# Optimization experiments

Measured on AMD Instinct MI355X. Metric: run time of the kernel, lower is better.

## Reference

```python
import jax, jax.numpy as jnp
import numpy as np

EPSILON = 0.1        # SinkhornConfig.epsilon
NUM_INNER_ITER = 10  # SinkhornConfig.num_inner_iter
STAB = 1e-8          # denominator stabilizer from forward()


def setup_inputs() -> dict:
    key = jax.random.key(0)
    k1, k2 = jax.random.split(key)
    source_features = jax.random.uniform(k1, (8192, 64), dtype=jnp.float32)
    target_features = jax.random.uniform(k2, (8192, 64), dtype=jnp.float32)
    return {"source_features": source_features, "target_features": target_features}


def _cost_matrix(s, t):
    # pairwise Euclidean distance ||s_i - t_j||_2, computed without the
    # [Ns, Nt, D] broadcast the torch code materializes (same math).
    s2 = jnp.sum(s * s, axis=1, keepdims=True)          # [Ns, 1]
    t2 = jnp.sum(t * t, axis=1, keepdims=True).T        # [1, Nt]
    sq = s2 + t2 - 2.0 * (s @ t.T)                      # [Ns, Nt]
    return jnp.sqrt(jnp.maximum(sq, 0.0))


def reference(source_features, target_features):
    ns = source_features.shape[0]
    nt = target_features.shape[0]
    # uniform weights, normalized (source_weights/target_weights is None path)
    sw = jnp.full((ns, 1), 1.0 / ns, dtype=source_features.dtype)
    tw = jnp.full((nt, 1), 1.0 / nt, dtype=target_features.dtype)

    cost = _cost_matrix(source_features, target_features)   # [Ns, Nt]
    kernel = jnp.exp(-cost / EPSILON)                        # Gibbs kernel

    u = jnp.ones((ns, 1), dtype=cost.dtype)
    v = jnp.ones((nt, 1), dtype=cost.dtype)
    for _ in range(NUM_INNER_ITER):  # fixed small trip count
        u = sw / (kernel @ v + STAB)
        v = tw / (kernel.T @ u + STAB)

    coupling = u * kernel * v.T                              # [Ns, Nt]
    sinkhorn_dist = jnp.sum(coupling * cost) / (ns * nt)     # reduction='mean'
    return sinkhorn_dist, coupling, u, v
```

## Files before the change

kernel.cpp:

```cpp
#include <hip/hip_runtime.h>
#include <hip/hip_bf16.h>
#include <math.h>

#define NSRC 8192
#define NTGT 8192
#define DIM 64

typedef short bf16x8 __attribute__((ext_vector_type(8)));
typedef float f32x16 __attribute__((ext_vector_type(16)));

__device__ __forceinline__ float wave_reduce_sum(float x) {
#pragma unroll
  for (int off = 32; off > 0; off >>= 1) x += __shfl_down(x, off, 64);
  return x;
}

__device__ __forceinline__ float bflo(unsigned int u) {
  return __uint_as_float(u << 16);
}
__device__ __forceinline__ float bfhi(unsigned int u) {
  return __uint_as_float(u & 0xFFFF0000u);
}
__device__ __forceinline__ unsigned short f2bfr(float x) {
  __hip_bfloat16 b = __float2bfloat16(x);
  return __hip_bfloat16_raw(b).x;
}

__global__ __launch_bounds__(256) void norms_k(const float* __restrict__ S,
                                               const float* __restrict__ T,
                                               float* __restrict__ s2,
                                               float* __restrict__ t2) {
  int i = blockIdx.x * 256 + threadIdx.x;
  if (i >= NSRC + NTGT) return;
  const float* base = (i < NSRC) ? (S + (size_t)i * DIM)
                                 : (T + (size_t)(i - NSRC) * DIM);
  const float4* p = (const float4*)base;
  float a = 0.f;
#pragma unroll
  for (int k = 0; k < DIM / 4; ++k) {
    float4 v = p[k];
    a += v.x * v.x + v.y * v.y + v.z * v.z + v.w * v.w;
  }
  if (i < NSRC) s2[i] = a;
  else          t2[i - NSRC] = a;
}

__global__ __launch_bounds__(256) void prep_k(const float* __restrict__ S,
                                              const float* __restrict__ T,
                                              unsigned short* __restrict__ Shi,
                                              unsigned short* __restrict__ Slo,
                                              unsigned short* __restrict__ Thi,
                                              unsigned short* __restrict__ Tlo) {
  int i = blockIdx.x * 256 + threadIdx.x;
  const float* src;
  unsigned short *dh, *dl;
  if (i < 65536) { src = S; dh = Shi; dl = Slo; }
  else { src = T; dh = Thi; dl = Tlo; i -= 65536; }
  const float4* p = (const float4*)(src + (size_t)i * 8);
  float4 x = p[0], y = p[1];
  float vals[8] = {x.x, x.y, x.z, x.w, y.x, y.y, y.z, y.w};
  unsigned int h[8], lo[8];
#pragma unroll
  for (int e = 0; e < 8; ++e) {
    unsigned short hr = f2bfr(vals[e]);
    h[e] = hr;
    lo[e] = f2bfr(vals[e] - bflo(hr));
  }
  uint4 hw = make_uint4(h[0] | (h[1] << 16), h[2] | (h[3] << 16),
                        h[4] | (h[5] << 16), h[6] | (h[7] << 16));
  uint4 lw = make_uint4(lo[0] | (lo[1] << 16), lo[2] | (lo[3] << 16),
                        lo[4] | (lo[5] << 16), lo[6] | (lo[7] << 16));
  *(uint4*)(dh + (size_t)i * 8) = hw;
  *(uint4*)(dl + (size_t)i * 8) = lw;
}

__global__ __launch_bounds__(256) void init_k(float* __restrict__ c,
                                              float* __restrict__ v_out,
                                              float* __restrict__ rowacc) {
  int i = blockIdx.x * 256 + threadIdx.x;
  if (i < NTGT) {
    c[i] = 0.f;
    v_out[i] = 1.f;
    rowacc[i] = 0.f;
  }
}

#define PR(r) ((((r) >> 3) + (((r)&7) << 3)))

__global__ __launch_bounds__(256) void kbuild_mfma_k(
    const unsigned short* __restrict__ Shi, const unsigned short* __restrict__ Slo,
    const unsigned short* __restrict__ Thi, const unsigned short* __restrict__ Tlo,
    const float* __restrict__ s2, const float* __restrict__ t2,
    __hip_bfloat16* __restrict__ Kb, __hip_bfloat16* __restrict__ KbT,
    float* __restrict__ rowacc) {
  __shared__ unsigned short sAh[64][72], sAl[64][72];
  __shared__ unsigned short sBh[64][72], sBl[64][72];
  __shared__ unsigned short stage[64][72];
  __shared__ float sS2[64], sT2[64];

  const int tid = threadIdx.x;
  const int bm = blockIdx.y * 64, bn = blockIdx.x * 64;

#pragma unroll
  for (int p = 0; p < 2; ++p) {
    int f = tid + 256 * p;
    int row = f >> 3, seg = (f & 7) * 8;
    *(uint4*)&sAh[row][seg] = ((const uint4*)(Shi + (size_t)bm * DIM))[f];
    *(uint4*)&sAl[row][seg] = ((const uint4*)(Slo + (size_t)bm * DIM))[f];
    *(uint4*)&sBh[row][seg] = ((const uint4*)(Thi + (size_t)bn * DIM))[f];
    *(uint4*)&sBl[row][seg] = ((const uint4*)(Tlo + (size_t)bn * DIM))[f];
  }
  if (tid < 64) sS2[tid] = s2[bm + tid];
  else if (tid < 128) sT2[tid - 64] = t2[bn + (tid - 64)];
  __syncthreads();

  const int w = tid >> 6, l = tid & 63;
  const int wr = w >> 1, wc = w & 1;
  const int arow = 32 * wr + (l & 31);
  const int brow = 32 * wc + (l & 31);
  const int kh = 8 * (l >> 5);

  f32x16 acc;
#pragma unroll
  for (int i = 0; i < 16; ++i) acc[i] = 0.f;

#pragma unroll
  for (int ks = 0; ks < 4; ++ks) {
    int ko = 16 * ks + kh;
    bf16x8 ah = *(const bf16x8*)&sAh[arow][ko];
    bf16x8 al = *(const bf16x8*)&sAl[arow][ko];
    bf16x8 bh = *(const bf16x8*)&sBh[brow][ko];
    bf16x8 bl = *(const bf16x8*)&sBl[brow][ko];
    acc = __builtin_amdgcn_mfma_f32_32x32x16_bf16(ah, bh, acc, 0, 0, 0);
    acc = __builtin_amdgcn_mfma_f32_32x32x16_bf16(ah, bl, acc, 0, 0, 0);
    acc = __builtin_amdgcn_mfma_f32_32x32x16_bf16(al, bh, acc, 0, 0, 0);
  }

#pragma unroll
  for (int j = 0; j < 16; ++j) {
    int rl = (j & 3) + 8 * (j >> 2) + 4 * (l >> 5);
    int row = 32 * wr + rl, col = 32 * wc + (l & 31);
    float sq = sS2[row] + sT2[col] - 2.f * acc[j];
    float kv = __expf(-10.f * sqrtf(fmaxf(sq, 0.f)));
    stage[PR(row)][col] = f2bfr(kv);
  }
  __syncthreads();

  {
    int row = tid >> 2, q = tid & 3;
    float a = 0.f;
#pragma unroll
    for (int m = 0; m < 16; ++m)
      a += bflo((unsigned int)stage[PR(row)][16 * q + m]);
    a += __shfl_down(a, 1, 4);
    a += __shfl_down(a, 2, 4);
    if (q == 0) atomicAdd(&rowacc[bm + row], a);
  }

#pragma unroll
  for (int p = 0; p < 2; ++p) {
    int f = tid + 256 * p;
    int row = f >> 3, seg = (f & 7) * 8;
    *(uint4*)(Kb + (size_t)(bm + row) * NTGT + bn + seg) =
        *(const uint4*)&stage[PR(row)][seg];
  }
#pragma unroll
  for (int p = 0; p < 2; ++p) {
    int f = tid + 256 * p;
    int tcol = f >> 3, gro = f & 7;
    unsigned int wds[4];
#pragma unroll
    for (int e = 0; e < 4; ++e) {
      unsigned int a0 = stage[gro + 8 * (2 * e)][tcol];
      unsigned int a1 = stage[gro + 8 * (2 * e + 1)][tcol];
      wds[e] = a0 | (a1 << 16);
    }
    *(uint4*)(KbT + (size_t)(bn + tcol) * NSRC + bm + 8 * gro) =
        make_uint4(wds[0], wds[1], wds[2], wds[3]);
  }
}

__global__ __launch_bounds__(256) void initu_k(const float* __restrict__ rowacc,
                                               float* __restrict__ u) {
  int i = blockIdx.x * 256 + threadIdx.x;
  u[i] = (1.0f / NSRC) / (rowacc[i] + 1e-8f);
}

__global__ __launch_bounds__(256) void rowsum_k(const unsigned short* __restrict__ P,
                                                const float* __restrict__ x,
                                                float* __restrict__ y) {
  int row = blockIdx.x * 4 + (threadIdx.x >> 6);
  int lane = threadIdx.x & 63;
  const uint4* r4 = (const uint4*)(P + (size_t)row * NTGT);
  const float4* x4 = (const float4*)x;
  float a = 0.f;
#pragma unroll 4
  for (int s = lane; s < NTGT / 8; s += 64) {
    uint4 q = r4[s];
    float4 xa = x4[2 * s], xb = x4[2 * s + 1];
    a += bflo(q.x) * xa.x + bfhi(q.x) * xa.y
       + bflo(q.y) * xa.z + bfhi(q.y) * xa.w
       + bflo(q.z) * xb.x + bfhi(q.z) * xb.y
       + bflo(q.w) * xb.z + bfhi(q.w) * xb.w;
  }
  a = wave_reduce_sum(a);
  if (lane == 0) y[row] = (1.0f / 8192.0f) / (a + 1e-8f);
}

__global__ __launch_bounds__(256) void coupling_bf16_k(
    const unsigned short* __restrict__ Kb,
    const float* __restrict__ u,
    const float* __restrict__ v,
    float* __restrict__ C,
    float* __restrict__ partials) {
  __shared__ float red[4];
  size_t g = (size_t)blockIdx.x * 256 + threadIdx.x;
  size_t base = g * 32;
  int i = (int)(base >> 13);
  int j0 = (int)(base & 8191);
  float ui = u[i];
  const uint4* kp = (const uint4*)(Kb + base);
  const float4* vp = (const float4*)(v + j0);
  float part = 0.f;
#pragma unroll
  for (int s = 0; s < 4; ++s) {
    uint4 q = kp[s];
    float4 va = vp[2 * s], vb = vp[2 * s + 1];
    float k0 = bflo(q.x), k1 = bfhi(q.x), k2 = bflo(q.y), k3 = bfhi(q.y);
    float k4 = bflo(q.z), k5 = bfhi(q.z), k6 = bflo(q.w), k7 = bfhi(q.w);
    float c0 = ui * k0 * va.x, c1 = ui * k1 * va.y;
    float c2 = ui * k2 * va.z, c3 = ui * k3 * va.w;
    float c4 = ui * k4 * vb.x, c5 = ui * k5 * vb.y;
    float c6 = ui * k6 * vb.z, c7 = ui * k7 * vb.w;
    part += c0 * __logf(fmaxf(k0, 1e-37f)) + c1 * __logf(fmaxf(k1, 1e-37f)) +
            c2 * __logf(fmaxf(k2, 1e-37f)) + c3 * __logf(fmaxf(k3, 1e-37f)) +
            c4 * __logf(fmaxf(k4, 1e-37f)) + c5 * __logf(fmaxf(k5, 1e-37f)) +
            c6 * __logf(fmaxf(k6, 1e-37f)) + c7 * __logf(fmaxf(k7, 1e-37f));
    float* cw = C + base + 8 * s;
    *(float4*)cw       = make_float4(c0, c1, c2, c3);
    *(float4*)(cw + 4) = make_float4(c4, c5, c6, c7);
  }
  part = wave_reduce_sum(part);
  int wid = threadIdx.x >> 6, lane = threadIdx.x & 63;
  if (lane == 0) red[wid] = part;
  __syncthreads();
  if (threadIdx.x == 0)
    partials[blockIdx.x] = red[0] + red[1] + red[2] + red[3];
}

#define BM 64
#define BN 128
__global__ __launch_bounds__(256) void kbuild_k(const float* __restrict__ S,
                                                const float* __restrict__ T,
                                                const float* __restrict__ s2,
                                                const float* __restrict__ t2,
                                                float* __restrict__ Kf) {
  __shared__ float sT[BM][68];
  __shared__ float tT[BN][68];
  const int bn = blockIdx.x * BN;
  const int bm = blockIdx.y * BM;
  const int tid = threadIdx.x;
  {
    const float4* sg = (const float4*)(S + (size_t)bm * DIM);
#pragma unroll
    for (int k = 0; k < 4; ++k) {
      int f = tid + 256 * k;
      int row = f >> 4, c4 = f & 15;
      *(float4*)&sT[row][c4 * 4] = sg[f];
    }
    const float4* tg = (const float4*)(T + (size_t)bn * DIM);
#pragma unroll
    for (int k = 0; k < 8; ++k) {
      int f = tid + 256 * k;
      int row = f >> 4, c4 = f & 15;
      *(float4*)&tT[row][c4 * 4] = tg[f];
    }
  }
  __syncthreads();
  const int tx = tid & 15;
  const int ty = tid >> 4;
  float acc[4][8];
#pragma unroll
  for (int a = 0; a < 4; ++a)
#pragma unroll
    for (int b = 0; b < 8; ++b) acc[a][b] = 0.f;
  for (int k = 0; k < DIM; k += 4) {
    float4 sr[4], trg[8];
#pragma unroll
    for (int a = 0; a < 4; ++a) sr[a] = *(float4*)&sT[ty + 16 * a][k];
#pragma unroll
    for (int b = 0; b < 8; ++b) trg[b] = *(float4*)&tT[tx + 16 * b][k];
#pragma unroll
    for (int a = 0; a < 4; ++a)
#pragma unroll
      for (int b = 0; b < 8; ++b) {
        acc[a][b] += sr[a].x * trg[b].x;
        acc[a][b] += sr[a].y * trg[b].y;
        acc[a][b] += sr[a].z * trg[b].z;
        acc[a][b] += sr[a].w * trg[b].w;
      }
  }
#pragma unroll
  for (int a = 0; a < 4; ++a) {
    int gi = bm + ty + 16 * a;
    float s2v = s2[gi];
#pragma unroll
    for (int b = 0; b < 8; ++b) {
      int gj = bn + tx + 16 * b;
      float sq = s2v + t2[gj] - 2.f * acc[a][b];
      float cost = sqrtf(fmaxf(sq, 0.f));
      Kf[(size_t)gi * NTGT + gj] = __expf(-10.f * cost);
    }
  }
}

__global__ __launch_bounds__(256) void rowsum_f32_k(const float* __restrict__ K,
                                                    const float* __restrict__ v,
                                                    float* __restrict__ u_out) {
  int row = (blockIdx.x * 256 + threadIdx.x) >> 6;
  int lane = threadIdx.x & 63;
  const float4* r4 = (const float4*)(K + (size_t)row * NTGT);
  const float4* v4 = (const float4*)v;
  float a = 0.f;
#pragma unroll 4
  for (int j = lane; j < NTGT / 4; j += 64) {
    float4 k4 = r4[j];
    float4 vv = v4[j];
    a += k4.x * vv.x + k4.y * vv.y + k4.z * vv.z + k4.w * vv.w;
  }
  a = wave_reduce_sum(a);
  if (lane == 0) u_out[row] = (1.0f / NSRC) / (a + 1e-8f);
}

__global__ __launch_bounds__(256) void colsum_f32_k(const float* __restrict__ K,
                                                    const float* __restrict__ u,
                                                    float* __restrict__ c) {
  int j = blockIdx.x * 1024 + threadIdx.x * 4;
  int i0 = blockIdx.y * 64;
  float a0 = 0.f, a1 = 0.f, a2 = 0.f, a3 = 0.f;
#pragma unroll 8
  for (int i = i0; i < i0 + 64; ++i) {
    float ui = u[i];
    float4 k4 = *(const float4*)(K + (size_t)i * NTGT + j);
    a0 += k4.x * ui; a1 += k4.y * ui; a2 += k4.z * ui; a3 += k4.w * ui;
  }
  atomicAdd(&c[j + 0], a0);
  atomicAdd(&c[j + 1], a1);
  atomicAdd(&c[j + 2], a2);
  atomicAdd(&c[j + 3], a3);
}

__global__ __launch_bounds__(256) void finishv_k(float* __restrict__ c,
                                                 float* __restrict__ v_out) {
  int j = blockIdx.x * 256 + threadIdx.x;
  v_out[j] = (1.0f / NTGT) / (c[j] + 1e-8f);
  c[j] = 0.f;
}

__global__ __launch_bounds__(256) void coupling_f32_k(float* __restrict__ K,
                                                      const float* __restrict__ u,
                                                      const float* __restrict__ v,
                                                      float* __restrict__ partials) {
  __shared__ float red[4];
  size_t t0 = (size_t)blockIdx.x * 2048 + threadIdx.x;
  float part = 0.f;
#pragma unroll
  for (int s = 0; s < 8; ++s) {
    size_t f4 = t0 + (size_t)s * 256;
    size_t base = f4 * 4;
    int i = (int)(base >> 13);
    int j = (int)(base & 8191);
    float4 k4 = *(float4*)(K + base);
    float ui = u[i];
    float4 vv = *(const float4*)(v + j);
    float c0 = ui * k4.x * vv.x;
    float c1 = ui * k4.y * vv.y;
    float c2 = ui * k4.z * vv.z;
    float c3 = ui * k4.w * vv.w;
    part += c0 * __logf(k4.x) + c1 * __logf(k4.y) +
            c2 * __logf(k4.z) + c3 * __logf(k4.w);
    *(float4*)(K + base) = make_float4(c0, c1, c2, c3);
  }
  part = wave_reduce_sum(part);
  int wid = threadIdx.x >> 6, lane = threadIdx.x & 63;
  if (lane == 0) red[wid] = part;
  __syncthreads();
  if (threadIdx.x == 0)
    partials[blockIdx.x] = red[0] + red[1] + red[2] + red[3];
}

__global__ __launch_bounds__(256) void finalize_k(const float* __restrict__ partials,
                                                  float* __restrict__ out) {
  __shared__ float red[4];
  float a = 0.f;
  for (int i = threadIdx.x; i < 8192; i += 256) a += partials[i];
  a = wave_reduce_sum(a);
  int wid = threadIdx.x >> 6, lane = threadIdx.x & 63;
  if (lane == 0) red[wid] = a;
  __syncthreads();
  if (threadIdx.x == 0)
    out[0] = (red[0] + red[1] + red[2] + red[3]) *
             (-0.1f / ((float)NSRC * (float)NTGT));
}

extern "C" void kernel_launch(void* const* d_in, const int* in_sizes, int n_in,
                              void* d_out, int out_size, void* d_ws, size_t ws_size,
                              hipStream_t stream) {
  const float* S = (const float*)d_in[0];
  const float* T = (const float*)d_in[1];
  float* out = (float*)d_out;

  float* C  = out + 1;
  float* u  = out + 1 + (size_t)NSRC * NTGT;
  float* vv = u + NSRC;

  __hip_bfloat16* KbT = (__hip_bfloat16*)C;

  char* wsb = (char*)d_ws;
  float* s2       = (float*)(wsb);
  float* t2       = (float*)(wsb + (32 << 10));
  float* partials = (float*)(wsb + (64 << 10));
  float* c        = (float*)(wsb + (96 << 10));
  float* rowacc   = (float*)(wsb + (128 << 10));
  unsigned short* Shi = (unsigned short*)(wsb + (1 << 20));
  unsigned short* Slo = (unsigned short*)(wsb + (2 << 20));
  unsigned short* Thi = (unsigned short*)(wsb + (3 << 20));
  unsigned short* Tlo = (unsigned short*)(wsb + (4 << 20));
  const size_t KB_OFF = (size_t)8 << 20;
  const size_t KB_BYTES = (size_t)NSRC * NTGT * 2;
  __hip_bfloat16* Kb = (__hip_bfloat16*)(wsb + KB_OFF);

  bool full = ws_size >= KB_OFF + KB_BYTES;

  norms_k<<<(NSRC + NTGT + 255) / 256, 256, 0, stream>>>(S, T, s2, t2);

  if (full) {
    prep_k<<<512, 256, 0, stream>>>(S, T, Shi, Slo, Thi, Tlo);
    init_k<<<NTGT / 256, 256, 0, stream>>>(c, vv, rowacc);
    kbuild_mfma_k<<<dim3(128, 128), 256, 0, stream>>>(
        Shi, Slo, Thi, Tlo, s2, t2, Kb, KbT, rowacc);
    initu_k<<<NSRC / 256, 256, 0, stream>>>(rowacc, u);
    for (int it = 0; it < 10; ++it) {
      if (it > 0)
        rowsum_k<<<NSRC / 4, 256, 0, stream>>>((const unsigned short*)Kb, vv, u);
      rowsum_k<<<NTGT / 4, 256, 0, stream>>>((const unsigned short*)KbT, u, vv);
    }
    coupling_bf16_k<<<8192, 256, 0, stream>>>(
        (const unsigned short*)Kb, u, vv, C, partials);
  } else {
    init_k<<<NTGT / 256, 256, 0, stream>>>(c, vv, partials );
    kbuild_k<<<dim3(NTGT / BN, NSRC / BM), 256, 0, stream>>>(S, T, s2, t2, C);
    for (int it = 0; it < 10; ++it) {
      rowsum_f32_k<<<NSRC * 64 / 256, 256, 0, stream>>>(C, vv, u);
      colsum_f32_k<<<dim3(8, 128), 256, 0, stream>>>(C, u, c);
      finishv_k<<<NTGT / 256, 256, 0, stream>>>(c, vv);
    }
    coupling_f32_k<<<8192, 256, 0, stream>>>(C, u, vv, partials);
  }
  finalize_k<<<1, 256, 0, stream>>>(partials, out);
}
```

Before: 686.2 us.

## Drop transposed bf16 kernel copy; compute column sums from Kb with split partials

The Gibbs kernel is no longer stored a second time in transposed form. The v-update now reads the row-major Kb directly: colsum_part_k writes per-16-row-chunk column partials and csum1v_k reduces the 512 partials into v. Row sums from the build kernel are written as per-block partials instead of atomics, and the workspace layout is changed to hold the partial buffers. This removes 128MB of transposed writes and the strided LDS transpose, but each iteration now writes and reads a 16MB partial buffer.

```diff
diff --git a/kernel.cpp b/kernel.cpp
--- a/kernel.cpp
+++ b/kernel.cpp
@@ -75,24 +75,19 @@
 }
 
 __global__ __launch_bounds__(256) void init_k(float* __restrict__ c,
-                                              float* __restrict__ v_out,
-                                              float* __restrict__ rowacc) {
+                                              float* __restrict__ v_out) {
   int i = blockIdx.x * 256 + threadIdx.x;
   if (i < NTGT) {
     c[i] = 0.f;
     v_out[i] = 1.f;
-    rowacc[i] = 0.f;
-  }
-}
-
-#define PR(r) ((((r) >> 3) + (((r)&7) << 3)))
+  }
+}
 
 __global__ __launch_bounds__(256) void kbuild_mfma_k(
     const unsigned short* __restrict__ Shi, const unsigned short* __restrict__ Slo,
     const unsigned short* __restrict__ Thi, const unsigned short* __restrict__ Tlo,
     const float* __restrict__ s2, const float* __restrict__ t2,
-    __hip_bfloat16* __restrict__ Kb, __hip_bfloat16* __restrict__ KbT,
-    float* __restrict__ rowacc) {
+    __hip_bfloat16* __restrict__ Kb, float* __restrict__ rowpart) {
   __shared__ unsigned short sAh[64][72], sAl[64][72];
   __shared__ unsigned short sBh[64][72], sBl[64][72];
   __shared__ unsigned short stage[64][72];
@@ -142,7 +137,7 @@
     int row = 32 * wr + rl, col = 32 * wc + (l & 31);
     float sq = sS2[row] + sT2[col] - 2.f * acc[j];
     float kv = __expf(-10.f * sqrtf(fmaxf(sq, 0.f)));
-    stage[PR(row)][col] = f2bfr(kv);
+    stage[row][col] = f2bfr(kv);
   }
   __syncthreads();
 
@@ -151,10 +146,10 @@
     float a = 0.f;
 #pragma unroll
     for (int m = 0; m < 16; ++m)
-      a += bflo((unsigned int)stage[PR(row)][16 * q + m]);
+      a += bflo((unsigned int)stage[row][16 * q + m]);
     a += __shfl_down(a, 1, 4);
     a += __shfl_down(a, 2, 4);
-    if (q == 0) atomicAdd(&rowacc[bm + row], a);
+    if (q == 0) rowpart[(size_t)blockIdx.x * NSRC + bm + row] = a;
   }
 
 #pragma unroll
@@ -162,28 +157,17 @@
     int f = tid + 256 * p;
     int row = f >> 3, seg = (f & 7) * 8;
     *(uint4*)(Kb + (size_t)(bm + row) * NTGT + bn + seg) =
-        *(const uint4*)&stage[PR(row)][seg];
-  }
-#pragma unroll
-  for (int p = 0; p < 2; ++p) {
-    int f = tid + 256 * p;
-    int tcol = f >> 3, gro = f & 7;
-    unsigned int wds[4];
-#pragma unroll
-    for (int e = 0; e < 4; ++e) {
-      unsigned int a0 = stage[gro + 8 * (2 * e)][tcol];
-      unsigned int a1 = stage[gro + 8 * (2 * e + 1)][tcol];
-      wds[e] = a0 | (a1 << 16);
-    }
-    *(uint4*)(KbT + (size_t)(bn + tcol) * NSRC + bm + 8 * gro) =
-        make_uint4(wds[0], wds[1], wds[2], wds[3]);
-  }
-}
-
-__global__ __launch_bounds__(256) void initu_k(const float* __restrict__ rowacc,
+        *(const uint4*)&stage[row][seg];
+  }
+}
+
+__global__ __launch_bounds__(256) void initu_k(const float* __restrict__ rowpart,
                                                float* __restrict__ u) {
   int i = blockIdx.x * 256 + threadIdx.x;
-  u[i] = (1.0f / NSRC) / (rowacc[i] + 1e-8f);
+  float a = 0.f;
+#pragma unroll 8
+  for (int bn = 0; bn < 128; ++bn) a += rowpart[(size_t)bn * NSRC + i];
+  u[i] = (1.0f / NSRC) / (a + 1e-8f);
 }
 
 __global__ __launch_bounds__(256) void rowsum_k(const unsigned short* __restrict__ P,
@@ -207,6 +191,62 @@
   if (lane == 0) y[row] = (1.0f / 8192.0f) / (a + 1e-8f);
 }
 
+__global__ __launch_bounds__(256) void colsum_part_k(
+    const unsigned short* __restrict__ Kb,
+    const float* __restrict__ u,
+    float* __restrict__ c_part) {
+  const int ic = blockIdx.x;
+  const int t = threadIdx.x;
+  const uint4* kp = (const uint4*)(Kb + (size_t)ic * 16 * NTGT);
+
+  float acc[32];
+#pragma unroll
+  for (int k = 0; k < 32; ++k) acc[k] = 0.f;
+
+#pragma unroll 4
+  for (int r = 0; r < 16; ++r) {
+    float ui = u[16 * ic + r];
+    uint4 q0 = kp[r * 1024 + 0 * 256 + t];
+    uint4 q1 = kp[r * 1024 + 1 * 256 + t];
+    uint4 q2 = kp[r * 1024 + 2 * 256 + t];
+    uint4 q3 = kp[r * 1024 + 3 * 256 + t];
+    acc[0]  += bflo(q0.x) * ui; acc[1]  += bfhi(q0.x) * ui;
+    acc[2]  += bflo(q0.y) * ui; acc[3]  += bfhi(q0.y) * ui;
+    acc[4]  += bflo(q0.z) * ui; acc[5]  += bfhi(q0.z) * ui;
+    acc[6]  += bflo(q0.w) * ui; acc[7]  += bfhi(q0.w) * ui;
+    acc[8]  += bflo(q1.x) * ui; acc[9]  += bfhi(q1.x) * ui;
+    acc[10] += bflo(q1.y) * ui; acc[11] += bfhi(q1.y) * ui;
+    acc[12] += bflo(q1.z) * ui; acc[13] += bfhi(q1.z) * ui;
+    acc[14] += bflo(q1.w) * ui; acc[15] += bfhi(q1.w) * ui;
+    acc[16] += bflo(q2.x) * ui; acc[17] += bfhi(q2.x) * ui;
+    acc[18] += bflo(q2.y) * ui; acc[19] += bfhi(q2.y) * ui;
+    acc[20] += bflo(q2.z) * ui; acc[21] += bfhi(q2.z) * ui;
+    acc[22] += bflo(q2.w) * ui; acc[23] += bfhi(q2.w) * ui;
+    acc[24] += bflo(q3.x) * ui; acc[25] += bfhi(q3.x) * ui;
+    acc[26] += bflo(q3.y) * ui; acc[27] += bfhi(q3.y) * ui;
+    acc[28] += bflo(q3.z) * ui; acc[29] += bfhi(q3.z) * ui;
+    acc[30] += bflo(q3.w) * ui; acc[31] += bfhi(q3.w) * ui;
+  }
+
+  float* dst = c_part + (size_t)ic * NTGT + 8 * t;
+#pragma unroll
+  for (int s = 0; s < 4; ++s) {
+    *(float4*)(dst + 2048 * s)     = make_float4(acc[8 * s + 0], acc[8 * s + 1],
+                                                 acc[8 * s + 2], acc[8 * s + 3]);
+    *(float4*)(dst + 2048 * s + 4) = make_float4(acc[8 * s + 4], acc[8 * s + 5],
+                                                 acc[8 * s + 6], acc[8 * s + 7]);
+  }
+}
+
+__global__ __launch_bounds__(256) void csum1v_k(const float* __restrict__ c_part,
+                                                float* __restrict__ v_out) {
+  int j = blockIdx.x * 256 + threadIdx.x;
+  float a = 0.f;
+#pragma unroll 8
+  for (int ic = 0; ic < 512; ++ic) a += c_part[(size_t)ic * NTGT + j];
+  v_out[j] = (1.0f / NTGT) / (a + 1e-8f);
+}
+
 __global__ __launch_bounds__(256) void coupling_bf16_k(
     const unsigned short* __restrict__ Kb,
     const float* __restrict__ u,
@@ -414,41 +454,42 @@
   float* u  = out + 1 + (size_t)NSRC * NTGT;
   float* vv = u + NSRC;
 
-  __hip_bfloat16* KbT = (__hip_bfloat16*)C;
-
   char* wsb = (char*)d_ws;
   float* s2       = (float*)(wsb);
   float* t2       = (float*)(wsb + (32 << 10));
   float* partials = (float*)(wsb + (64 << 10));
   float* c        = (float*)(wsb + (96 << 10));
-  float* rowacc   = (float*)(wsb + (128 << 10));
-  unsigned short* Shi = (unsigned short*)(wsb + (1 << 20));
-  unsigned short* Slo = (unsigned short*)(wsb + (2 << 20));
-  unsigned short* Thi = (unsigned short*)(wsb + (3 << 20));
-  unsigned short* Tlo = (unsigned short*)(wsb + (4 << 20));
-  const size_t KB_OFF = (size_t)8 << 20;
+  const size_t KB_OFF = 512 << 10;
   const size_t KB_BYTES = (size_t)NSRC * NTGT * 2;
+  const size_t CP_OFF = KB_OFF + KB_BYTES;
+  const size_t CP_BYTES = (size_t)512 * NTGT * 4;
   __hip_bfloat16* Kb = (__hip_bfloat16*)(wsb + KB_OFF);
-
-  bool full = ws_size >= KB_OFF + KB_BYTES;
+  float* c_part = (float*)(wsb + CP_OFF);
+  unsigned short* Shi = (unsigned short*)(wsb + CP_OFF);
+  unsigned short* Slo = (unsigned short*)(wsb + CP_OFF + (1 << 20));
+  unsigned short* Thi = (unsigned short*)(wsb + CP_OFF + (2 << 20));
+  unsigned short* Tlo = (unsigned short*)(wsb + CP_OFF + (3 << 20));
+  float* rowpart = (float*)(wsb + CP_OFF + (4 << 20));
+
+  bool full = ws_size >= CP_OFF + CP_BYTES;
 
   norms_k<<<(NSRC + NTGT + 255) / 256, 256, 0, stream>>>(S, T, s2, t2);
+  init_k<<<NTGT / 256, 256, 0, stream>>>(c, vv);
 
   if (full) {
     prep_k<<<512, 256, 0, stream>>>(S, T, Shi, Slo, Thi, Tlo);
-    init_k<<<NTGT / 256, 256, 0, stream>>>(c, vv, rowacc);
     kbuild_mfma_k<<<dim3(128, 128), 256, 0, stream>>>(
-        Shi, Slo, Thi, Tlo, s2, t2, Kb, KbT, rowacc);
-    initu_k<<<NSRC / 256, 256, 0, stream>>>(rowacc, u);
+        Shi, Slo, Thi, Tlo, s2, t2, Kb, rowpart);
+    initu_k<<<NSRC / 256, 256, 0, stream>>>(rowpart, u);
     for (int it = 0; it < 10; ++it) {
       if (it > 0)
         rowsum_k<<<NSRC / 4, 256, 0, stream>>>((const unsigned short*)Kb, vv, u);
-      rowsum_k<<<NTGT / 4, 256, 0, stream>>>((const unsigned short*)KbT, u, vv);
+      colsum_part_k<<<512, 256, 0, stream>>>((const unsigned short*)Kb, u, c_part);
+      csum1v_k<<<NTGT / 256, 256, 0, stream>>>(c_part, vv);
     }
     coupling_bf16_k<<<8192, 256, 0, stream>>>(
         (const unsigned short*)Kb, u, vv, C, partials);
   } else {
-    init_k<<<NTGT / 256, 256, 0, stream>>>(c, vv, partials );
     kbuild_k<<<dim3(NTGT / BN, NSRC / BM), 256, 0, stream>>>(S, T, s2, t2, C);
     for (int it = 0; it < 10; ++it) {
       rowsum_f32_k<<<NSRC * 64 / 256, 256, 0, stream>>>(C, vv, u);
```

Result: slower. 860.7 us (+25.4%).

## Recompute cost via MFMA in coupling pass and replace row-sum atomics with partials

Applied to the files above, without the earlier changes.

The coupling kernel no longer reads the stored bf16 Gibbs matrix. It recomputes the distance tile with split-bf16 MFMA and writes the coupling and the cost-weighted partial sums directly. This removes a full read of the large matrix at the price of extra matrix math per tile. The row-sum atomics in the kernel build are replaced by per-block partial writes that initu_k reduces, which also drops the init launch. The rowsum unroll factor goes from 4 to 8.

```diff
diff --git a/kernel.cpp b/kernel.cpp
--- a/kernel.cpp
+++ b/kernel.cpp
@@ -75,13 +75,11 @@
 }
 
 __global__ __launch_bounds__(256) void init_k(float* __restrict__ c,
-                                              float* __restrict__ v_out,
-                                              float* __restrict__ rowacc) {
+                                              float* __restrict__ v_out) {
   int i = blockIdx.x * 256 + threadIdx.x;
   if (i < NTGT) {
     c[i] = 0.f;
     v_out[i] = 1.f;
-    rowacc[i] = 0.f;
   }
 }
 
@@ -92,7 +90,7 @@
     const unsigned short* __restrict__ Thi, const unsigned short* __restrict__ Tlo,
     const float* __restrict__ s2, const float* __restrict__ t2,
     __hip_bfloat16* __restrict__ Kb, __hip_bfloat16* __restrict__ KbT,
-    float* __restrict__ rowacc) {
+    float* __restrict__ rowpart) {
   __shared__ unsigned short sAh[64][72], sAl[64][72];
   __shared__ unsigned short sBh[64][72], sBl[64][72];
   __shared__ unsigned short stage[64][72];
@@ -154,7 +152,7 @@
       a += bflo((unsigned int)stage[PR(row)][16 * q + m]);
     a += __shfl_down(a, 1, 4);
     a += __shfl_down(a, 2, 4);
-    if (q == 0) atomicAdd(&rowacc[bm + row], a);
+    if (q == 0) rowpart[(size_t)blockIdx.x * NSRC + bm + row] = a;
   }
 
 #pragma unroll
@@ -180,10 +178,13 @@
   }
 }
 
-__global__ __launch_bounds__(256) void initu_k(const float* __restrict__ rowacc,
+__global__ __launch_bounds__(256) void initu_k(const float* __restrict__ rowpart,
                                                float* __restrict__ u) {
   int i = blockIdx.x * 256 + threadIdx.x;
-  u[i] = (1.0f / NSRC) / (rowacc[i] + 1e-8f);
+  float a = 0.f;
+#pragma unroll 8
+  for (int bn = 0; bn < 128; ++bn) a += rowpart[(size_t)bn * NSRC + i];
+  u[i] = (1.0f / NSRC) / (a + 1e-8f);
 }
 
 __global__ __launch_bounds__(256) void rowsum_k(const unsigned short* __restrict__ P,
@@ -194,7 +195,7 @@
   const uint4* r4 = (const uint4*)(P + (size_t)row * NTGT);
   const float4* x4 = (const float4*)x;
   float a = 0.f;
-#pragma unroll 4
+#pragma unroll 8
   for (int s = lane; s < NTGT / 8; s += 64) {
     uint4 q = r4[s];
     float4 xa = x4[2 * s], xb = x4[2 * s + 1];
@@ -207,45 +208,74 @@
   if (lane == 0) y[row] = (1.0f / 8192.0f) / (a + 1e-8f);
 }
 
-__global__ __launch_bounds__(256) void coupling_bf16_k(
-    const unsigned short* __restrict__ Kb,
-    const float* __restrict__ u,
-    const float* __restrict__ v,
-    float* __restrict__ C,
-    float* __restrict__ partials) {
+__global__ __launch_bounds__(256) void coupling_rc_k(
+    const unsigned short* __restrict__ Shi, const unsigned short* __restrict__ Slo,
+    const unsigned short* __restrict__ Thi, const unsigned short* __restrict__ Tlo,
+    const float* __restrict__ s2, const float* __restrict__ t2,
+    const float* __restrict__ u, const float* __restrict__ v,
+    float* __restrict__ C, float* __restrict__ partials) {
+  __shared__ unsigned short sAh[64][72], sAl[64][72];
+  __shared__ unsigned short sBh[64][72], sBl[64][72];
+  __shared__ float sS2[64], sT2[64], sU[64], sV[64];
   __shared__ float red[4];
-  size_t g = (size_t)blockIdx.x * 256 + threadIdx.x;
-  size_t base = g * 32;
-  int i = (int)(base >> 13);
-  int j0 = (int)(base & 8191);
-  float ui = u[i];
-  const uint4* kp = (const uint4*)(Kb + base);
-  const float4* vp = (const float4*)(v + j0);
+
+  const int tid = threadIdx.x;
+  const int bm = blockIdx.y * 64, bn = blockIdx.x * 64;
+
+#pragma unroll
+  for (int p = 0; p < 2; ++p) {
+    int f = tid + 256 * p;
+    int row = f >> 3, seg = (f & 7) * 8;
+    *(uint4*)&sAh[row][seg] = ((const uint4*)(Shi + (size_t)bm * DIM))[f];
+    *(uint4*)&sAl[row][seg] = ((const uint4*)(Slo + (size_t)bm * DIM))[f];
+    *(uint4*)&sBh[row][seg] = ((const uint4*)(Thi + (size_t)bn * DIM))[f];
+    *(uint4*)&sBl[row][seg] = ((const uint4*)(Tlo + (size_t)bn * DIM))[f];
+  }
+  if (tid < 64)       sS2[tid] = s2[bm + tid];
+  else if (tid < 128) sT2[tid - 64] = t2[bn + (tid - 64)];
+  else if (tid < 192) sU[tid - 128] = u[bm + (tid - 128)];
+  else                sV[tid - 192] = v[bn + (tid - 192)];
+  __syncthreads();
+
+  const int w = tid >> 6, l = tid & 63;
+  const int wr = w >> 1, wc = w & 1;
+  const int arow = 32 * wr + (l & 31);
+  const int brow = 32 * wc + (l & 31);
+  const int kh = 8 * (l >> 5);
+
+  f32x16 acc;
+#pragma unroll
+  for (int i = 0; i < 16; ++i) acc[i] = 0.f;
+
+#pragma unroll
+  for (int ks = 0; ks < 4; ++ks) {
+    int ko = 16 * ks + kh;
+    bf16x8 ah = *(const bf16x8*)&sAh[arow][ko];
+    bf16x8 al = *(const bf16x8*)&sAl[arow][ko];
+    bf16x8 bh = *(const bf16x8*)&sBh[brow][ko];
+    bf16x8 bl = *(const bf16x8*)&sBl[brow][ko];
+    acc = __builtin_amdgcn_mfma_f32_32x32x16_bf16(ah, bh, acc, 0, 0, 0);
+    acc = __builtin_amdgcn_mfma_f32_32x32x16_bf16(ah, bl, acc, 0, 0, 0);
+    acc = __builtin_amdgcn_mfma_f32_32x32x16_bf16(al, bh, acc, 0, 0, 0);
+  }
+
   float part = 0.f;
 #pragma unroll
-  for (int s = 0; s < 4; ++s) {
-    uint4 q = kp[s];
-    float4 va = vp[2 * s], vb = vp[2 * s + 1];
-    float k0 = bflo(q.x), k1 = bfhi(q.x), k2 = bflo(q.y), k3 = bfhi(q.y);
-    float k4 = bflo(q.z), k5 = bfhi(q.z), k6 = bflo(q.w), k7 = bfhi(q.w);
-    float c0 = ui * k0 * va.x, c1 = ui * k1 * va.y;
-    float c2 = ui * k2 * va.z, c3 = ui * k3 * va.w;
-    float c4 = ui * k4 * vb.x, c5 = ui * k5 * vb.y;
-    float c6 = ui * k6 * vb.z, c7 = ui * k7 * vb.w;
-    part += c0 * __logf(fmaxf(k0, 1e-37f)) + c1 * __logf(fmaxf(k1, 1e-37f)) +
-            c2 * __logf(fmaxf(k2, 1e-37f)) + c3 * __logf(fmaxf(k3, 1e-37f)) +
-            c4 * __logf(fmaxf(k4, 1e-37f)) + c5 * __logf(fmaxf(k5, 1e-37f)) +
-            c6 * __logf(fmaxf(k6, 1e-37f)) + c7 * __logf(fmaxf(k7, 1e-37f));
-    float* cw = C + base + 8 * s;
-    *(float4*)cw       = make_float4(c0, c1, c2, c3);
-    *(float4*)(cw + 4) = make_float4(c4, c5, c6, c7);
+  for (int j = 0; j < 16; ++j) {
+    int rl = (j & 3) + 8 * (j >> 2) + 4 * (l >> 5);
+    int row = 32 * wr + rl, col = 32 * wc + (l & 31);
+    float sq = sS2[row] + sT2[col] - 2.f * acc[j];
+    float cost = sqrtf(fmaxf(sq, 0.f));
+    float kv = __expf(-10.f * cost);
+    float cpl = sU[row] * kv * sV[col];
+    C[(size_t)(bm + row) * NTGT + bn + col] = cpl;
+    part += cpl * cost;
   }
   part = wave_reduce_sum(part);
-  int wid = threadIdx.x >> 6, lane = threadIdx.x & 63;
-  if (lane == 0) red[wid] = part;
-  __syncthreads();
-  if (threadIdx.x == 0)
-    partials[blockIdx.x] = red[0] + red[1] + red[2] + red[3];
+  if (l == 0) red[w] = part;
+  __syncthreads();
+  if (tid == 0)
+    partials[blockIdx.y * 128 + blockIdx.x] = red[0] + red[1] + red[2] + red[3];
 }
 
 #define BM 64
@@ -390,17 +420,18 @@
 }
 
 __global__ __launch_bounds__(256) void finalize_k(const float* __restrict__ partials,
-                                                  float* __restrict__ out) {
+                                                  float* __restrict__ out,
+                                                  int npart, float scale) {
   __shared__ float red[4];
   float a = 0.f;
-  for (int i = threadIdx.x; i < 8192; i += 256) a += partials[i];
+  for (int i = threadIdx.x; i < npart; i += 256) a += partials[i];
   a = wave_reduce_sum(a);
   int wid = threadIdx.x >> 6, lane = threadIdx.x & 63;
   if (lane == 0) red[wid] = a;
   __syncthreads();
   if (threadIdx.x == 0)
     out[0] = (red[0] + red[1] + red[2] + red[3]) *
-             (-0.1f / ((float)NSRC * (float)NTGT));
+             (scale / ((float)NSRC * (float)NTGT));
 }
 
 extern "C" void kernel_launch(void* const* d_in, const int* in_sizes, int n_in,
@@ -419,14 +450,14 @@
   char* wsb = (char*)d_ws;
   float* s2       = (float*)(wsb);
   float* t2       = (float*)(wsb + (32 << 10));
-  float* partials = (float*)(wsb + (64 << 10));
-  float* c        = (float*)(wsb + (96 << 10));
-  float* rowacc   = (float*)(wsb + (128 << 10));
-  unsigned short* Shi = (unsigned short*)(wsb + (1 << 20));
-  unsigned short* Slo = (unsigned short*)(wsb + (2 << 20));
-  unsigned short* Thi = (unsigned short*)(wsb + (3 << 20));
-  unsigned short* Tlo = (unsigned short*)(wsb + (4 << 20));
-  const size_t KB_OFF = (size_t)8 << 20;
+  float* c        = (float*)(wsb + (64 << 10));
+  float* partials = (float*)(wsb + (128 << 10));
+  float* rowpart  = (float*)(wsb + (1 << 20));
+  unsigned short* Shi = (unsigned short*)(wsb + ((size_t)6 << 20));
+  unsigned short* Slo = (unsigned short*)(wsb + ((size_t)7 << 20));
+  unsigned short* Thi = (unsigned short*)(wsb + ((size_t)8 << 20));
+  unsigned short* Tlo = (unsigned short*)(wsb + ((size_t)9 << 20));
+  const size_t KB_OFF = (size_t)16 << 20;
   const size_t KB_BYTES = (size_t)NSRC * NTGT * 2;
   __hip_bfloat16* Kb = (__hip_bfloat16*)(wsb + KB_OFF);
 
@@ -436,19 +467,19 @@
 
   if (full) {
     prep_k<<<512, 256, 0, stream>>>(S, T, Shi, Slo, Thi, Tlo);
-    init_k<<<NTGT / 256, 256, 0, stream>>>(c, vv, rowacc);
     kbuild_mfma_k<<<dim3(128, 128), 256, 0, stream>>>(
-        Shi, Slo, Thi, Tlo, s2, t2, Kb, KbT, rowacc);
-    initu_k<<<NSRC / 256, 256, 0, stream>>>(rowacc, u);
+        Shi, Slo, Thi, Tlo, s2, t2, Kb, KbT, rowpart);
+    initu_k<<<NSRC / 256, 256, 0, stream>>>(rowpart, u);
     for (int it = 0; it < 10; ++it) {
       if (it > 0)
         rowsum_k<<<NSRC / 4, 256, 0, stream>>>((const unsigned short*)Kb, vv, u);
       rowsum_k<<<NTGT / 4, 256, 0, stream>>>((const unsigned short*)KbT, u, vv);
     }
-    coupling_bf16_k<<<8192, 256, 0, stream>>>(
-        (const unsigned short*)Kb, u, vv, C, partials);
+    coupling_rc_k<<<dim3(128, 128), 256, 0, stream>>>(
+        Shi, Slo, Thi, Tlo, s2, t2, u, vv, C, partials);
+    finalize_k<<<1, 256, 0, stream>>>(partials, out, 16384, 1.0f);
   } else {
-    init_k<<<NTGT / 256, 256, 0, stream>>>(c, vv, partials );
+    init_k<<<NTGT / 256, 256, 0, stream>>>(c, vv);
     kbuild_k<<<dim3(NTGT / BN, NSRC / BM), 256, 0, stream>>>(S, T, s2, t2, C);
     for (int it = 0; it < 10; ++it) {
       rowsum_f32_k<<<NSRC * 64 / 256, 256, 0, stream>>>(C, vv, u);
@@ -456,6 +487,6 @@
       finishv_k<<<NTGT / 256, 256, 0, stream>>>(c, vv);
     }
     coupling_f32_k<<<8192, 256, 0, stream>>>(C, u, vv, partials);
-  }
-  finalize_k<<<1, 256, 0, stream>>>(partials, out);
-}
+    finalize_k<<<1, 256, 0, stream>>>(partials, out, 8192, -0.1f);
+  }
+}
```

Measured after the change: 722.2 us. +5.3%, slower.
